# Optimization experiments

Measured on AMD Instinct MI355X. Metric: run time of the kernel, lower is better.

The kernel has to match this reference:

```python
import jax, jax.numpy as jnp
import numpy as np

D_CH = 2048  # channels
N = 64       # hidden_state
L = 8192     # sequence length
MIN_DELTA, MAX_DELTA = 1e-3, 0.1


def setup_inputs() -> dict:
    key = jax.random.key(0)
    ks = jax.random.split(key, 5)
    X = jax.random.normal(ks[0], (D_CH, L), jnp.float32)
    # kaiming_normal_(nonlinearity='linear'): std = 1/sqrt(fan_in=N)
    A = jax.random.normal(ks[1], (N, N), jnp.float32) * (1.0 / N) ** 0.5
    B = jax.random.normal(ks[2], (N, D_CH), jnp.float32) * (1.0 / N) ** 0.5
    C = jax.random.normal(ks[3], (D_CH, N), jnp.float32)
    Dp = jnp.ones((D_CH,), jnp.float32)
    log_delta = jax.random.uniform(ks[4], (1,), jnp.float32,
                                   float(np.log(MIN_DELTA)), float(np.log(MAX_DELTA)))
    return {"X": X, "A": A, "B": B, "C": C, "Dp": Dp, "log_delta": log_delta}


def reference(X, A, B, C, Dp, log_delta):
    # X: (D, L). Bilinear (Tustin) discretization with dt = exp(log_delta).
    n = A.shape[0]
    delta = jnp.exp(log_delta)[0]
    I = jnp.eye(n, dtype=A.dtype)
    inv = jnp.linalg.inv(I - (delta * 0.5) * A)
    dA = inv @ (I + (delta * 0.5) * A)      # (N, N)
    dB = delta * (inv @ B)                   # (N, D)

    def step(h, x_t):
        # h: (N,), x_t: (D,)
        h = dA @ h + dB @ x_t
        return h, C @ h                      # y_t: (D,)

    h0 = jnp.zeros((n,), X.dtype)
    _, ys = jax.lax.scan(step, h0, X.T)      # ys: (L, D)
    # skip connection y += D * X (per-channel)
    return ys.T + Dp[:, None] * X            # (D, L)
```

## Files before the change

### kernel.cpp

```cpp
#include <hip/hip_runtime.h>
#include <math.h>

#define D_CH 2048
#define LSEQ 8192
#define T1 32
#define NC1 256
#define VSLAB 524288

typedef __attribute__((ext_vector_type(8))) short bf16x8;
typedef __attribute__((ext_vector_type(4))) float f32x4;

__device__ __forceinline__ short f2bf(float x) {
  unsigned u = __float_as_uint(x);
  u += 0x7FFFu + ((u >> 16) & 1);
  return (short)(u >> 16);
}

__device__ __forceinline__ void mmzero(float acc[16]) {
#pragma unroll
  for (int t = 0; t < 16; ++t) acc[t] = 0.f;
}

template <int SZ>
__device__ __forceinline__ void mmld(float acc[16], const float* __restrict__ Z,
                                     int r0, int c0) {
#pragma unroll
  for (int i = 0; i < 4; ++i) {
    float4 z = *(const float4*)&Z[(r0 + i) * SZ + c0];
    acc[i * 4 + 0] = z.x; acc[i * 4 + 1] = z.y;
    acc[i * 4 + 2] = z.z; acc[i * 4 + 3] = z.w;
  }
}

template <int SX, int SY>
__device__ __forceinline__ void mac44(float acc[16], const float* __restrict__ Xb,
                                      const float* __restrict__ Yb, int r0, int c0) {
#pragma unroll 4
  for (int k = 0; k < 64; k += 4) {
    float4 x0 = *(const float4*)&Xb[(r0 + 0) * SX + k];
    float4 x1 = *(const float4*)&Xb[(r0 + 1) * SX + k];
    float4 x2 = *(const float4*)&Xb[(r0 + 2) * SX + k];
    float4 x3 = *(const float4*)&Xb[(r0 + 3) * SX + k];
    float4 y0 = *(const float4*)&Yb[(k + 0) * SY + c0];
    float4 y1 = *(const float4*)&Yb[(k + 1) * SY + c0];
    float4 y2 = *(const float4*)&Yb[(k + 2) * SY + c0];
    float4 y3 = *(const float4*)&Yb[(k + 3) * SY + c0];
#define MROW(i, xi) \
    acc[i * 4 + 0] += xi.x * y0.x + xi.y * y1.x + xi.z * y2.x + xi.w * y3.x; \
    acc[i * 4 + 1] += xi.x * y0.y + xi.y * y1.y + xi.z * y2.y + xi.w * y3.y; \
    acc[i * 4 + 2] += xi.x * y0.z + xi.y * y1.z + xi.z * y2.z + xi.w * y3.z; \
    acc[i * 4 + 3] += xi.x * y0.w + xi.y * y1.w + xi.z * y2.w + xi.w * y3.w;
    MROW(0, x0) MROW(1, x1) MROW(2, x2) MROW(3, x3)
#undef MROW
  }
}

template <int SZ>
__device__ __forceinline__ void mmst(float* Dst, const float acc[16], int r0, int c0) {
#pragma unroll
  for (int i = 0; i < 4; ++i)
    *(float4*)&Dst[(r0 + i) * SZ + c0] =
        make_float4(acc[i * 4 + 0], acc[i * 4 + 1], acc[i * 4 + 2], acc[i * 4 + 3]);
}

__global__ __launch_bounds__(256) void main_kernel(const float* __restrict__ X,
                                                   const float* __restrict__ A,
                                                   const float* __restrict__ B,
                                                   const float* __restrict__ logd,
                                                   float* __restrict__ invdT,
                                                   float* __restrict__ dAg,
                                                   float* __restrict__ V,
                                                   int KS) {
  __shared__ float smem[8704];
  const int tid = threadIdx.x;
  const int lane = tid & 63;
  const int w = tid >> 6;

  if (blockIdx.x == 0) {
    float* bQ = smem;
    float* bP = smem + 4352;
    const int r0 = (tid >> 4) * 4, c0 = (tid & 15) * 4;
    const float delta = expf(logd[0]);
    const float half = 0.5f * delta;
    float accQ[16], accP[16];

    for (int idx = tid; idx < 4096; idx += 256) {
      int i = idx >> 6, j = idx & 63;
      float p = half * A[idx];
      bP[i * 68 + j] = p;
      bQ[i * 68 + j] = p + (i == j ? 1.f : 0.f);
    }
    __syncthreads();
    mmzero(accP); mac44<68, 68>(accP, bP, bP, r0, c0);
    __syncthreads();
    mmst<68>(bP, accP, r0, c0);
    __syncthreads();
#pragma unroll 1
    for (int s = 0; s < 3; ++s) {
      mmld<68>(accQ, bQ, r0, c0);
      mac44<68, 68>(accQ, bP, bQ, r0, c0);
      if (s < 2) { mmzero(accP); mac44<68, 68>(accP, bP, bP, r0, c0); }
      __syncthreads();
      mmst<68>(bQ, accQ, r0, c0);
      if (s < 2) mmst<68>(bP, accP, r0, c0);
      __syncthreads();
    }

    for (int idx = tid; idx < 4096; idx += 256) {
      int n = idx >> 6, m = idx & 63;
      float qv = bQ[n * 68 + m];
      invdT[m * 64 + n] = delta * qv;
      dAg[idx] = 2.f * qv - (n == m ? 1.f : 0.f);
    }
    return;
  }

  const int b = blockIdx.x - 1;
  const int t0 = (b & 255) << 5;
  const int slab = b >> 8;
  const int k0 = slab * KS;
  short* Xs = (short*)smem;
  short* Bs = (short*)smem + 2304;
  const int q = lane >> 4, r = lane & 15;
  const int hi = lane >> 5, tl = lane & 31;
  const int brow = lane >> 3;
  const int bkc = (lane & 7) * 8;
  const int wm = (w & 1) * 16;
  const int wn = (w >> 1) * 32;

  f32x4 acc[2];
#pragma unroll
  for (int j = 0; j < 2; ++j) acc[j] = (f32x4){0.f, 0.f, 0.f, 0.f};

  float xv[8];
  float bv[16];

#define LOADX(KK)                                                              \
  _Pragma("unroll")                                                            \
  for (int j = 0; j < 8; ++j)                                                  \
    xv[j] = X[(size_t)(k0 + (KK) + w * 16 + hi * 8 + j) * LSEQ + t0 + tl];

#define LOADB(KK)                                                              \
  _Pragma("unroll")                                                            \
  for (int p = 0; p < 2; ++p) {                                                \
    int n = p * 32 + w * 8 + brow;                                             \
    float4 f0 = *(const float4*)&B[(size_t)n * D_CH + k0 + (KK) + bkc];        \
    float4 f1 = *(const float4*)&B[(size_t)n * D_CH + k0 + (KK) + bkc + 4];    \
    bv[p * 8 + 0] = f0.x; bv[p * 8 + 1] = f0.y;                                \
    bv[p * 8 + 2] = f0.z; bv[p * 8 + 3] = f0.w;                                \
    bv[p * 8 + 4] = f1.x; bv[p * 8 + 5] = f1.y;                                \
    bv[p * 8 + 6] = f1.z; bv[p * 8 + 7] = f1.w;                                \
  }

  LOADX(0)
  LOADB(0)

  for (int kk = 0; kk < KS; kk += 64) {
    bf16x8 xp;
#pragma unroll
    for (int j = 0; j < 8; ++j) xp[j] = f2bf(xv[j]);
    *(bf16x8*)&Xs[tl * 72 + w * 16 + hi * 8] = xp;
#pragma unroll
    for (int p = 0; p < 2; ++p) {
      bf16x8 bp8;
#pragma unroll
      for (int j = 0; j < 8; ++j) bp8[j] = f2bf(bv[p * 8 + j]);
      *(bf16x8*)&Bs[(p * 32 + w * 8 + brow) * 72 + bkc] = bp8;
    }
    __syncthreads();

    if (kk + 64 < KS) {
      LOADX(kk + 64)
      LOADB(kk + 64)
    }

#pragma unroll
    for (int ks = 0; ks < 64; ks += 32) {
      bf16x8 a = *(const bf16x8*)&Xs[(wm + r) * 72 + ks + q * 8];
#pragma unroll
      for (int j = 0; j < 2; ++j) {
        bf16x8 bb = *(const bf16x8*)&Bs[(wn + j * 16 + r) * 72 + ks + q * 8];
        acc[j] = __builtin_amdgcn_mfma_f32_16x16x32_bf16(a, bb, acc[j], 0, 0, 0);
      }
    }
    __syncthreads();
  }
#undef LOADX
#undef LOADB

  float* Vs = V + (size_t)slab * VSLAB;
#pragma unroll
  for (int j = 0; j < 2; ++j)
#pragma unroll
    for (int reg = 0; reg < 4; ++reg)
      Vs[(size_t)(t0 + wm + q * 4 + reg) * 64 + wn + j * 16 + r] = acc[j][reg];
}

__device__ __forceinline__ float matvec(const float ar[64], const float* __restrict__ hb,
                                        float u) {
  float a0 = u, a1 = 0.f, a2 = 0.f, a3 = 0.f;
#pragma unroll
  for (int jj = 0; jj < 64; jj += 4) {
    float4 hv = *(const float4*)&hb[jj];
    a0 += ar[jj + 0] * hv.x;
    a1 += ar[jj + 1] * hv.y;
    a2 += ar[jj + 2] * hv.z;
    a3 += ar[jj + 3] * hv.w;
  }
  return (a0 + a1) + (a2 + a3);
}

__global__ __launch_bounds__(256) void scan1_kernel(const float* __restrict__ V,
                                                    const float* __restrict__ invdT,
                                                    const float* __restrict__ dA,
                                                    float* __restrict__ U,
                                                    float* __restrict__ S,
                                                    float* __restrict__ dA32g,
                                                    float* __restrict__ dA512g,
                                                    int nslab) {
  __shared__ float smem[8704];
  const int tid = threadIdx.x;
  const int c = blockIdx.x;

  if (c == NC1) {
    float* b0 = smem;
    float* b1 = smem + 4352;
    const int r0 = (tid >> 4) * 4, c0 = (tid & 15) * 4;
    for (int idx = tid; idx < 4096; idx += 256)
      b0[(idx >> 6) * 68 + (idx & 63)] = dA[idx];
    __syncthreads();
    float acc[16];
    float* p = b0; float* q = b1;
    for (int s = 1; s <= 9; ++s) {
      mmzero(acc); mac44<68, 68>(acc, p, p, r0, c0);
      if (s == 5) mmst<64>(dA32g, acc, r0, c0);
      if (s == 9) mmst<64>(dA512g, acc, r0, c0);
      mmst<68>(q, acc, r0, c0);
      __syncthreads();
      float* t = p; p = q; q = t;
    }
    return;
  }

  float* invs = smem;
  float* Vs   = smem + 4096;
  float* Us   = smem + 6144;
  float* hs0  = smem + 8192;
  float* hs1  = smem + 8256;

  for (int idx = tid; idx < 4096; idx += 256) invs[idx] = invdT[idx];
  for (int idx = tid; idx < 2048; idx += 256) {
    float v = 0.f;
    for (int s = 0; s < nslab; ++s) v += V[(size_t)s * VSLAB + (size_t)c * 2048 + idx];
    Vs[idx] = v;
  }
  __syncthreads();

  const int r0 = (tid >> 4) * 2, c0 = (tid & 15) * 4;
  float a0[4] = {0.f, 0.f, 0.f, 0.f}, a1[4] = {0.f, 0.f, 0.f, 0.f};
#pragma unroll 4
  for (int k = 0; k < 64; k += 4) {
    float4 v0 = *(const float4*)&Vs[r0 * 64 + k];
    float4 v1 = *(const float4*)&Vs[(r0 + 1) * 64 + k];
    float4 y0 = *(const float4*)&invs[(k + 0) * 64 + c0];
    float4 y1 = *(const float4*)&invs[(k + 1) * 64 + c0];
    float4 y2 = *(const float4*)&invs[(k + 2) * 64 + c0];
    float4 y3 = *(const float4*)&invs[(k + 3) * 64 + c0];
    a0[0] += v0.x * y0.x + v0.y * y1.x + v0.z * y2.x + v0.w * y3.x;
    a0[1] += v0.x * y0.y + v0.y * y1.y + v0.z * y2.y + v0.w * y3.y;
    a0[2] += v0.x * y0.z + v0.y * y1.z + v0.z * y2.z + v0.w * y3.z;
    a0[3] += v0.x * y0.w + v0.y * y1.w + v0.z * y2.w + v0.w * y3.w;
    a1[0] += v1.x * y0.x + v1.y * y1.x + v1.z * y2.x + v1.w * y3.x;
    a1[1] += v1.x * y0.y + v1.y * y1.y + v1.z * y2.y + v1.w * y3.y;
    a1[2] += v1.x * y0.z + v1.y * y1.z + v1.z * y2.z + v1.w * y3.z;
    a1[3] += v1.x * y0.w + v1.y * y1.w + v1.z * y2.w + v1.w * y3.w;
  }
  *(float4*)&Us[r0 * 64 + c0] = make_float4(a0[0], a0[1], a0[2], a0[3]);
  *(float4*)&Us[(r0 + 1) * 64 + c0] = make_float4(a1[0], a1[1], a1[2], a1[3]);
  *(float4*)&U[(size_t)(c * 32 + r0) * 64 + c0] = make_float4(a0[0], a0[1], a0[2], a0[3]);
  *(float4*)&U[(size_t)(c * 32 + r0 + 1) * 64 + c0] = make_float4(a1[0], a1[1], a1[2], a1[3]);
  __syncthreads();

  if (tid < 64) {
    float ar[64];
#pragma unroll
    for (int jj = 0; jj < 64; jj += 4) {
      float4 v = *(const float4*)&dA[tid * 64 + jj];
      ar[jj] = v.x; ar[jj + 1] = v.y; ar[jj + 2] = v.z; ar[jj + 3] = v.w;
    }
    float h = 0.f;
    hs0[tid] = 0.f;
    for (int t = 0; t < T1; ++t) {
      float u = Us[t * 64 + tid];
      h = matvec(ar, (t & 1) ? hs1 : hs0, u);
      ((t & 1) ? hs0 : hs1)[tid] = h;
    }
    S[c * 64 + tid] = h;
  }
}

__global__ __launch_bounds__(1024, 4) void mid_kernel(const float* __restrict__ S,
                                                      const float* __restrict__ dA32,
                                                      const float* __restrict__ dA512,
                                                      float* __restrict__ Hinit) {
  __shared__ float S2s[1024];
  __shared__ float H2s[1024];
  __shared__ float hsbuf[2048];
  const int tid = threadIdx.x;
  const int wave = tid >> 6, lane = tid & 63;
  float* hs0 = &hsbuf[wave * 128];
  float* hs1 = hs0 + 64;
  const float* inw = S + wave * 16 * 64;

  {
    float ar[64];
#pragma unroll
    for (int jj = 0; jj < 64; jj += 4) {
      float4 v = *(const float4*)&dA32[lane * 64 + jj];
      ar[jj] = v.x; ar[jj + 1] = v.y; ar[jj + 2] = v.z; ar[jj + 3] = v.w;
    }
    float h = 0.f;
    hs0[lane] = 0.f;
    for (int t = 0; t < 16; ++t) {
      float u = inw[t * 64 + lane];
      h = matvec(ar, (t & 1) ? hs1 : hs0, u);
      ((t & 1) ? hs0 : hs1)[lane] = h;
    }
    S2s[wave * 64 + lane] = h;
  }
  __syncthreads();

  if (wave == 0) {
    float br[64];
#pragma unroll
    for (int jj = 0; jj < 64; jj += 4) {
      float4 v = *(const float4*)&dA512[lane * 64 + jj];
      br[jj] = v.x; br[jj + 1] = v.y; br[jj + 2] = v.z; br[jj + 3] = v.w;
    }
    float g = 0.f;
    hs0[lane] = 0.f;
    for (int t = 0; t < 16; ++t) {
      H2s[t * 64 + lane] = g;
      float u = S2s[t * 64 + lane];
      g = matvec(br, (t & 1) ? hs1 : hs0, u);
      ((t & 1) ? hs0 : hs1)[lane] = g;
    }
  }
  __syncthreads();

  {
    float ar[64];
#pragma unroll
    for (int jj = 0; jj < 64; jj += 4) {
      float4 v = *(const float4*)&dA32[lane * 64 + jj];
      ar[jj] = v.x; ar[jj + 1] = v.y; ar[jj + 2] = v.z; ar[jj + 3] = v.w;
    }
    float h = H2s[wave * 64 + lane];
    hs0[lane] = h;
    for (int t = 0; t < 16; ++t) {
      Hinit[(wave * 16 + t) * 64 + lane] = h;
      float u = inw[t * 64 + lane];
      h = matvec(ar, (t & 1) ? hs1 : hs0, u);
      ((t & 1) ? hs0 : hs1)[lane] = h;
    }
  }
}

__global__ __launch_bounds__(64) void scan2_kernel(const float* __restrict__ U,
                                                   const float* __restrict__ dA,
                                                   const float* __restrict__ Hinit,
                                                   float* __restrict__ Ht) {
  __shared__ float hs[2][64];
  const int tid = threadIdx.x;
  const int c = blockIdx.x;
  float ar[64];
#pragma unroll
  for (int jj = 0; jj < 64; jj += 4) {
    float4 v = *(const float4*)&dA[tid * 64 + jj];
    ar[jj] = v.x; ar[jj + 1] = v.y; ar[jj + 2] = v.z; ar[jj + 3] = v.w;
  }
  float h = Hinit[c * 64 + tid];
  hs[0][tid] = h;
  const float* inc = U + (size_t)c * T1 * 64;
  float* outc = Ht + (size_t)c * T1 * 64;
  float up[4];
#pragma unroll
  for (int i = 0; i < 4; ++i) up[i] = inc[i * 64 + tid];

  for (int t = 0; t < T1; ++t) {
    float u = up[t & 3];
    if (t + 4 < T1) up[t & 3] = inc[(t + 4) * 64 + tid];
    h = matvec(ar, hs[t & 1], u);
    hs[(t + 1) & 1][tid] = h;
    outc[t * 64 + tid] = h;
  }
}

__global__ __launch_bounds__(256) void out_kernel(const float* __restrict__ X,
                                                  const float* __restrict__ C,
                                                  const float* __restrict__ Dp,
                                                  const float* __restrict__ Ht,
                                                  float* __restrict__ Y) {
  __shared__ short Cs[64 * 72];
  __shared__ short Hs[64 * 72];
  const int tid = threadIdx.x;
  const int lane = tid & 63, w = tid >> 6;
  const int t0 = blockIdx.x * 64;
  const int d0 = blockIdx.y * 64;
  const int q = lane >> 4, r = lane & 15;
  const int brow = lane >> 3, bkc = (lane & 7) * 8;

#pragma unroll
  for (int p = 0; p < 2; ++p) {
    int row = p * 32 + w * 8 + brow;
    float4 c0 = *(const float4*)&C[(size_t)(d0 + row) * 64 + bkc];
    float4 c1 = *(const float4*)&C[(size_t)(d0 + row) * 64 + bkc + 4];
    float4 h0 = *(const float4*)&Ht[(size_t)(t0 + row) * 64 + bkc];
    float4 h1 = *(const float4*)&Ht[(size_t)(t0 + row) * 64 + bkc + 4];
    bf16x8 cv, hv;
    cv[0] = f2bf(c0.x); cv[1] = f2bf(c0.y); cv[2] = f2bf(c0.z); cv[3] = f2bf(c0.w);
    cv[4] = f2bf(c1.x); cv[5] = f2bf(c1.y); cv[6] = f2bf(c1.z); cv[7] = f2bf(c1.w);
    hv[0] = f2bf(h0.x); hv[1] = f2bf(h0.y); hv[2] = f2bf(h0.z); hv[3] = f2bf(h0.w);
    hv[4] = f2bf(h1.x); hv[5] = f2bf(h1.y); hv[6] = f2bf(h1.z); hv[7] = f2bf(h1.w);
    *(bf16x8*)&Cs[row * 72 + bkc] = cv;
    *(bf16x8*)&Hs[row * 72 + bkc] = hv;
  }
  __syncthreads();

  f32x4 acc[4];
#pragma unroll
  for (int j = 0; j < 4; ++j) acc[j] = (f32x4){0.f, 0.f, 0.f, 0.f};
#pragma unroll
  for (int ks = 0; ks < 64; ks += 32) {
    bf16x8 a = *(const bf16x8*)&Cs[(w * 16 + r) * 72 + ks + q * 8];
#pragma unroll
    for (int j = 0; j < 4; ++j) {
      bf16x8 bb = *(const bf16x8*)&Hs[(j * 16 + r) * 72 + ks + q * 8];
      acc[j] = __builtin_amdgcn_mfma_f32_16x16x32_bf16(a, bb, acc[j], 0, 0, 0);
    }
  }

#pragma unroll
  for (int reg = 0; reg < 4; ++reg) {
    int d = d0 + w * 16 + q * 4 + reg;
    float dp = Dp[d];
#pragma unroll
    for (int j = 0; j < 4; ++j) {
      int t = t0 + j * 16 + r;
      size_t off = (size_t)d * LSEQ + t;
      Y[off] = acc[j][reg] + dp * X[off];
    }
  }
}

extern "C" void kernel_launch(void* const* d_in, const int* in_sizes, int n_in,
                              void* d_out, int out_size, void* d_ws, size_t ws_size,
                              hipStream_t stream) {
  const float* X  = (const float*)d_in[0];
  const float* A  = (const float*)d_in[1];
  const float* B  = (const float*)d_in[2];
  const float* Cm = (const float*)d_in[3];
  const float* Dp = (const float*)d_in[4];
  const float* ld = (const float*)d_in[5];
  float* out = (float*)d_out;
  float* ws = (float*)d_ws;

  const size_t need4 = (size_t)(16384 + 4 * VSLAB + VSLAB + 16384 + 16384) * 4;
  const int nslab = (ws_size >= need4) ? 4 : 2;

  float* invdT = ws;
  float* dA    = ws + 4096;
  float* dA32  = ws + 8192;
  float* dA512 = ws + 12288;
  float* V     = ws + 16384;
  float* U     = V + (size_t)nslab * VSLAB;
  float* S     = U + VSLAB;
  float* Hinit = S + 16384;
  float* Ht    = V;

  main_kernel<<<nslab * 256 + 1, 256, 0, stream>>>(X, A, B, ld, invdT, dA, V,
                                                   2048 / nslab);
  scan1_kernel<<<NC1 + 1, 256, 0, stream>>>(V, invdT, dA, U, S, dA32, dA512, nslab);
  mid_kernel<<<1, 1024, 0, stream>>>(S, dA32, dA512, Hinit);
  scan2_kernel<<<NC1, 64, 0, stream>>>(U, dA, Hinit, Ht);
  out_kernel<<<dim3(128, 32), 256, 0, stream>>>(X, Cm, Dp, Ht, out);
}
```

Baseline: 257.1 us.

## Read scan matrices from LDS and split mid kernel into three small launches

The sequential matvec scans now read the 64x64 transition matrix rows from padded shared memory instead of holding 64 floats per thread in registers. This cuts VGPR pressure and avoids possible spills. The single 1024-thread mid kernel, which ran a one-wave serial phase between two block-wide phases, becomes three separate kernels (16, 1 and 16 blocks) that pass intermediates through global workspace. In exchange, each matvec step adds LDS reads, there are two extra kernel launches, and the workspace grows.

After: 223.1 us. 13.2% less time.

```diff
diff --git a/kernel.cpp b/kernel.cpp
--- a/kernel.cpp
+++ b/kernel.cpp
@@ -196,18 +196,30 @@
       Vs[(size_t)(t0 + wm + q * 4 + reg) * 64 + wn + j * 16 + r] = acc[j][reg];
 }
 
-__device__ __forceinline__ float matvec(const float ar[64], const float* __restrict__ hb,
-                                        float u) {
+__device__ __forceinline__ float matvec_lds(const float* __restrict__ Mrow,
+                                            const float* __restrict__ hb, float u) {
   float a0 = u, a1 = 0.f, a2 = 0.f, a3 = 0.f;
 #pragma unroll
   for (int jj = 0; jj < 64; jj += 4) {
+    float4 m = *(const float4*)&Mrow[jj];
     float4 hv = *(const float4*)&hb[jj];
-    a0 += ar[jj + 0] * hv.x;
-    a1 += ar[jj + 1] * hv.y;
-    a2 += ar[jj + 2] * hv.z;
-    a3 += ar[jj + 3] * hv.w;
+    a0 += m.x * hv.x;
+    a1 += m.y * hv.y;
+    a2 += m.z * hv.z;
+    a3 += m.w * hv.w;
   }
   return (a0 + a1) + (a2 + a3);
+}
+
+__device__ __forceinline__ void stage_mat64(float* Mlds, const float* __restrict__ Mg,
+                                            int lane) {
+#pragma unroll
+  for (int i = 0; i < 16; ++i) {
+    int row = i * 4 + (lane >> 4);
+    int col = (lane & 15) * 4;
+    *(float4*)&Mlds[row * 68 + col] = *(const float4*)&Mg[row * 64 + col];
+  }
+  __syncthreads();
 }
 
 __global__ __launch_bounds__(256) void scan1_kernel(const float* __restrict__ V,
@@ -218,7 +230,7 @@
                                                     float* __restrict__ dA32g,
                                                     float* __restrict__ dA512g,
                                                     int nslab) {
-  __shared__ float smem[8704];
+  __shared__ float smem[13056];
   const int tid = threadIdx.x;
   const int c = blockIdx.x;
 
@@ -247,8 +259,11 @@
   float* Us   = smem + 6144;
   float* hs0  = smem + 8192;
   float* hs1  = smem + 8256;
+  float* Md   = smem + 8320;
 
   for (int idx = tid; idx < 4096; idx += 256) invs[idx] = invdT[idx];
+  for (int idx = tid; idx < 4096; idx += 256)
+    Md[(idx >> 6) * 68 + (idx & 63)] = dA[idx];
   for (int idx = tid; idx < 2048; idx += 256) {
     float v = 0.f;
     for (int s = 0; s < nslab; ++s) v += V[(size_t)s * VSLAB + (size_t)c * 2048 + idx];
@@ -282,87 +297,71 @@
   __syncthreads();
 
   if (tid < 64) {
-    float ar[64];
-#pragma unroll
-    for (int jj = 0; jj < 64; jj += 4) {
-      float4 v = *(const float4*)&dA[tid * 64 + jj];
-      ar[jj] = v.x; ar[jj + 1] = v.y; ar[jj + 2] = v.z; ar[jj + 3] = v.w;
-    }
+    const float* row = Md + tid * 68;
     float h = 0.f;
     hs0[tid] = 0.f;
     for (int t = 0; t < T1; ++t) {
       float u = Us[t * 64 + tid];
-      h = matvec(ar, (t & 1) ? hs1 : hs0, u);
+      h = matvec_lds(row, (t & 1) ? hs1 : hs0, u);
       ((t & 1) ? hs0 : hs1)[tid] = h;
     }
     S[c * 64 + tid] = h;
   }
 }
 
-__global__ __launch_bounds__(1024, 4) void mid_kernel(const float* __restrict__ S,
-                                                      const float* __restrict__ dA32,
-                                                      const float* __restrict__ dA512,
-                                                      float* __restrict__ Hinit) {
-  __shared__ float S2s[1024];
-  __shared__ float H2s[1024];
-  __shared__ float hsbuf[2048];
-  const int tid = threadIdx.x;
-  const int wave = tid >> 6, lane = tid & 63;
-  float* hs0 = &hsbuf[wave * 128];
-  float* hs1 = hs0 + 64;
-  const float* inw = S + wave * 16 * 64;
-
-  {
-    float ar[64];
-#pragma unroll
-    for (int jj = 0; jj < 64; jj += 4) {
-      float4 v = *(const float4*)&dA32[lane * 64 + jj];
-      ar[jj] = v.x; ar[jj + 1] = v.y; ar[jj + 2] = v.z; ar[jj + 3] = v.w;
-    }
-    float h = 0.f;
-    hs0[lane] = 0.f;
-    for (int t = 0; t < 16; ++t) {
-      float u = inw[t * 64 + lane];
-      h = matvec(ar, (t & 1) ? hs1 : hs0, u);
-      ((t & 1) ? hs0 : hs1)[lane] = h;
-    }
-    S2s[wave * 64 + lane] = h;
-  }
-  __syncthreads();
-
-  if (wave == 0) {
-    float br[64];
-#pragma unroll
-    for (int jj = 0; jj < 64; jj += 4) {
-      float4 v = *(const float4*)&dA512[lane * 64 + jj];
-      br[jj] = v.x; br[jj + 1] = v.y; br[jj + 2] = v.z; br[jj + 3] = v.w;
-    }
-    float g = 0.f;
-    hs0[lane] = 0.f;
-    for (int t = 0; t < 16; ++t) {
-      H2s[t * 64 + lane] = g;
-      float u = S2s[t * 64 + lane];
-      g = matvec(br, (t & 1) ? hs1 : hs0, u);
-      ((t & 1) ? hs0 : hs1)[lane] = g;
-    }
-  }
-  __syncthreads();
-
-  {
-    float ar[64];
-#pragma unroll
-    for (int jj = 0; jj < 64; jj += 4) {
-      float4 v = *(const float4*)&dA32[lane * 64 + jj];
-      ar[jj] = v.x; ar[jj + 1] = v.y; ar[jj + 2] = v.z; ar[jj + 3] = v.w;
-    }
-    float h = H2s[wave * 64 + lane];
-    hs0[lane] = h;
-    for (int t = 0; t < 16; ++t) {
-      Hinit[(wave * 16 + t) * 64 + lane] = h;
-      float u = inw[t * 64 + lane];
-      h = matvec(ar, (t & 1) ? hs1 : hs0, u);
-      ((t & 1) ? hs0 : hs1)[lane] = h;
-    }
+__global__ __launch_bounds__(64) void mid1_kernel(const float* __restrict__ S,
+                                                  const float* __restrict__ dA32,
+                                                  float* __restrict__ S2g) {
+  __shared__ float M[64 * 68];
+  __shared__ float hs[2][64];
+  const int lane = threadIdx.x;
+  const int g = blockIdx.x;
+  stage_mat64(M, dA32, lane);
+  const float* row = M + lane * 68;
+  const float* in = S + g * 16 * 64;
+  float h = 0.f;
+  hs[0][lane] = 0.f;
+  for (int t = 0; t < 16; ++t) {
+    h = matvec_lds(row, hs[t & 1], in[t * 64 + lane]);
+    hs[(t + 1) & 1][lane] = h;
+  }
+  S2g[g * 64 + lane] = h;
+}
+
+__global__ __launch_bounds__(64) void mid2_kernel(const float* __restrict__ S2g,
+                                                  const float* __restrict__ dA512,
+                                                  float* __restrict__ H2g) {
+  __shared__ float M[64 * 68];
+  __shared__ float hs[2][64];
+  const int lane = threadIdx.x;
+  stage_mat64(M, dA512, lane);
+  const float* row = M + lane * 68;
+  float h = 0.f;
+  hs[0][lane] = 0.f;
+  for (int t = 0; t < 16; ++t) {
+    H2g[t * 64 + lane] = h;
+    h = matvec_lds(row, hs[t & 1], S2g[t * 64 + lane]);
+    hs[(t + 1) & 1][lane] = h;
+  }
+}
+
+__global__ __launch_bounds__(64) void mid3_kernel(const float* __restrict__ S,
+                                                  const float* __restrict__ dA32,
+                                                  const float* __restrict__ H2g,
+                                                  float* __restrict__ Hinit) {
+  __shared__ float M[64 * 68];
+  __shared__ float hs[2][64];
+  const int lane = threadIdx.x;
+  const int g = blockIdx.x;
+  stage_mat64(M, dA32, lane);
+  const float* row = M + lane * 68;
+  const float* in = S + g * 16 * 64;
+  float h = H2g[g * 64 + lane];
+  hs[0][lane] = h;
+  for (int t = 0; t < 16; ++t) {
+    Hinit[(g * 16 + t) * 64 + lane] = h;
+    h = matvec_lds(row, hs[t & 1], in[t * 64 + lane]);
+    hs[(t + 1) & 1][lane] = h;
   }
 }
 
@@ -370,15 +369,12 @@
                                                    const float* __restrict__ dA,
                                                    const float* __restrict__ Hinit,
                                                    float* __restrict__ Ht) {
+  __shared__ float M[64 * 68];
   __shared__ float hs[2][64];
   const int tid = threadIdx.x;
   const int c = blockIdx.x;
-  float ar[64];
-#pragma unroll
-  for (int jj = 0; jj < 64; jj += 4) {
-    float4 v = *(const float4*)&dA[tid * 64 + jj];
-    ar[jj] = v.x; ar[jj + 1] = v.y; ar[jj + 2] = v.z; ar[jj + 3] = v.w;
-  }
+  stage_mat64(M, dA, tid);
+  const float* row = M + tid * 68;
   float h = Hinit[c * 64 + tid];
   hs[0][tid] = h;
   const float* inc = U + (size_t)c * T1 * 64;
@@ -390,7 +386,7 @@
   for (int t = 0; t < T1; ++t) {
     float u = up[t & 3];
     if (t + 4 < T1) up[t & 3] = inc[(t + 4) * 64 + tid];
-    h = matvec(ar, hs[t & 1], u);
+    h = matvec_lds(row, hs[t & 1], u);
     hs[(t + 1) & 1][tid] = h;
     outc[t * 64 + tid] = h;
   }
@@ -465,7 +461,8 @@
   float* out = (float*)d_out;
   float* ws = (float*)d_ws;
 
-  const size_t need4 = (size_t)(16384 + 4 * VSLAB + VSLAB + 16384 + 16384) * 4;
+  const size_t need4 =
+      (size_t)(16384 + 4 * VSLAB + VSLAB + 16384 + 16384 + 2048) * 4;
   const int nslab = (ws_size >= need4) ? 4 : 2;
 
   float* invdT = ws;
@@ -476,12 +473,16 @@
   float* U     = V + (size_t)nslab * VSLAB;
   float* S     = U + VSLAB;
   float* Hinit = S + 16384;
+  float* S2g   = Hinit + 16384;
+  float* H2g   = S2g + 1024;
   float* Ht    = V;
 
   main_kernel<<<nslab * 256 + 1, 256, 0, stream>>>(X, A, B, ld, invdT, dA, V,
                                                    2048 / nslab);
   scan1_kernel<<<NC1 + 1, 256, 0, stream>>>(V, invdT, dA, U, S, dA32, dA512, nslab);
-  mid_kernel<<<1, 1024, 0, stream>>>(S, dA32, dA512, Hinit);
+  mid1_kernel<<<16, 64, 0, stream>>>(S, dA32, S2g);
+  mid2_kernel<<<1, 64, 0, stream>>>(S2g, dA512, H2g);
+  mid3_kernel<<<16, 64, 0, stream>>>(S, dA32, H2g, Hinit);
   scan2_kernel<<<NC1, 64, 0, stream>>>(U, dA, Hinit, Ht);
   out_kernel<<<dim3(128, 32), 256, 0, stream>>>(X, Cm, Dp, Ht, out);
 }
```
